# Performance work log

Hardware: AMD Instinct MI355X
Metric: run time of the kernel (lower is better)

## Reference

```python
import jax, jax.numpy as jnp
import numpy as np

EPS = 1e-5
SCALE = 30.0

def _ln(x, g, b):
    m = jnp.mean(x, axis=-1, keepdims=True)
    v = jnp.mean((x - m) ** 2, axis=-1, keepdims=True)
    return (x - m) * jax.lax.rsqrt(v + EPS) * g + b

def setup_inputs() -> dict:
    key = jax.random.key(0)
    ks = jax.random.split(key, 12)
    B, L, K, H, NIN = 4, 2048, 48, 128, 512
    s = 0.02
    return {
        "h_V": jax.random.normal(ks[0], (B, L, H), jnp.float32),
        "h_E": jax.random.normal(ks[1], (B, L, K, NIN - H), jnp.float32),
        "mask_V": jnp.ones((B, L), jnp.float32),
        "mask_E": jnp.ones((B, L, K), jnp.float32),
        "w1": jax.random.normal(ks[2], (NIN, H), jnp.float32) * s,
        "b1": jnp.zeros((H,), jnp.float32),
        "w2": jax.random.normal(ks[3], (H, H), jnp.float32) * s,
        "b2": jnp.zeros((H,), jnp.float32),
        "w3": jax.random.normal(ks[4], (H, H), jnp.float32) * s,
        "b3": jnp.zeros((H,), jnp.float32),
        "g1": jnp.ones((H,), jnp.float32),
        "bn1": jnp.zeros((H,), jnp.float32),
        "g2": jnp.ones((H,), jnp.float32),
        "bn2": jnp.zeros((H,), jnp.float32),
        "wf1": jax.random.normal(ks[5], (H, 4 * H), jnp.float32) * s,
        "bf1": jnp.zeros((4 * H,), jnp.float32),
        "wf2": jax.random.normal(ks[6], (4 * H, H), jnp.float32) * s,
        "bf2": jnp.zeros((H,), jnp.float32),
    }

def reference(h_V, h_E, mask_V, mask_E, w1, b1, w2, b2, w3, b3, g1, bn1, g2, bn2, wf1, bf1, wf2, bf2):
    B, L, H = h_V.shape
    K = h_E.shape[-2]
    gelu = lambda x: jax.nn.gelu(x, approximate=False)  # torch nn.GELU default (erf)
    # expand source node over K neighbors and concat: (B,L,K,num_in)
    h_V_exp = jnp.broadcast_to(h_V[:, :, None, :], (B, L, K, H))
    h_EV = jnp.concatenate([h_V_exp, h_E], axis=-1)
    h_msg = gelu(jnp.einsum('blki,ih->blkh', h_EV, w1) + b1)
    h_msg = gelu(jnp.einsum('blkh,hj->blkj', h_msg, w2) + b2)
    h_msg = jnp.einsum('blkh,hj->blkj', h_msg, w3) + b3
    h_msg = mask_E[..., None] * h_msg
    dh = jnp.sum(h_msg, axis=-2) / SCALE  # masked sum-aggregate over K
    h = _ln(h_V + dh, g1, bn1)
    dff = jnp.einsum('blh,hf->blf', h, wf1) + bf1
    dff = jnp.einsum('blf,fh->blh', gelu(dff), wf2) + bf2
    h = _ln(h + dff, g2, bn2)
    return mask_V[..., None] * h
```

## Files before the change

kernel.cpp:

```cpp
#include <hip/hip_runtime.h>
#include <hip/hip_bf16.h>


typedef __bf16 bf16x8 __attribute__((ext_vector_type(8)));
typedef __bf16 bf16x4 __attribute__((ext_vector_type(4)));
typedef float f32x4 __attribute__((ext_vector_type(4)));

#define HH 128
#define EE 384
#define KK 48

__device__ __forceinline__ float gelu_f(float x) {
  float x2 = x * x;
  float u = x * (-1.5957691216f - 0.0713548163f * x2);
  float e = __expf(u);
  return __fdividef(x, 1.0f + e);
}

__device__ __forceinline__ bf16x8 cvt8v(f32x4 a, f32x4 b) {
  bf16x8 r;
  #pragma unroll
  for (int i = 0; i < 4; ++i) { r[i] = (__bf16)a[i]; r[i + 4] = (__bf16)b[i]; }
  return r;
}

__device__ __forceinline__ f32x4 mfma16(bf16x8 a, bf16x8 b, f32x4 c) {
  return __builtin_amdgcn_mfma_f32_16x16x32_bf16(a, b, c, 0, 0, 0);
}

__device__ __forceinline__ void gload16(const void* g, void* l) {
  __builtin_amdgcn_global_load_lds(
      (const __attribute__((address_space(1))) void*)g,
      (__attribute__((address_space(3))) void*)l, 16, 0, 0);
}

__global__ void prep_kernel(const float* __restrict__ w1, const float* __restrict__ w2,
                            const float* __restrict__ w3, const float* __restrict__ wf1,
                            const float* __restrict__ wf2, __bf16* __restrict__ out) {
  int idx = blockIdx.x * 256 + threadIdx.x;
  if (idx < 49152) {
    int t = idx & 7, lane = (idx >> 3) & 63, n = (idx >> 9) & 7, kc = idx >> 12;
    int e = kc * 32 + (lane >> 4) * 8 + t, h = n * 16 + (lane & 15);
    out[idx] = (__bf16)w1[(128 + e) * 128 + h];
  } else if (idx < 65536) {
    int u = idx - 49152;
    int t = u & 7, lane = (u >> 3) & 63, n = (u >> 9) & 7, kc = u >> 12;
    int e = kc * 32 + (lane >> 4) * 8 + t, h = n * 16 + (lane & 15);
    out[idx] = (__bf16)w2[e * 128 + h];
  } else if (idx < 81920) {
    int u = idx - 65536;
    int t = u & 7, lane = (u >> 3) & 63, n = (u >> 9) & 7, kc = u >> 12;
    int e = kc * 32 + (lane >> 4) * 8 + t, h = n * 16 + (lane & 15);
    out[idx] = (__bf16)w3[e * 128 + h];
  } else if (idx < 147456) {
    int u = idx - 81920;
    int t = u & 7, lane = (u >> 3) & 63, n = (u >> 9) & 7, kc = (u >> 12) & 3, w = u >> 14;
    int f = w * 128 + n * 16 + (lane & 15), h = kc * 32 + (lane >> 4) * 8 + t;
    out[idx] = (__bf16)wf1[h * 512 + f];
  } else if (idx < 212992) {
    int u = idx - 147456;
    int t = u & 7, lane = (u >> 3) & 63, n = (u >> 9) & 1, kc = (u >> 10) & 15, w = u >> 14;
    int j = w * 32 + n * 16 + (lane & 15), f = kc * 32 + (lane >> 4) * 8 + t;
    out[idx] = (__bf16)wf2[f * 128 + j];
  }
}

__global__ __launch_bounds__(128) void v1_kernel(const float* __restrict__ hV,
                                                 const float* __restrict__ w1,
                                                 const float* __restrict__ b1,
                                                 float* __restrict__ V1) {
  __shared__ __align__(16) float sV[16][128];
  const int tid = threadIdx.x;
  const long p0 = (long)blockIdx.x * 16;
  for (int i = 0; i < 16; ++i) sV[i][tid] = hV[(p0 + i) * HH + tid];
  __syncthreads();
  float acc[16];
  float bb = b1[tid];
  #pragma unroll
  for (int p = 0; p < 16; ++p) acc[p] = bb;
  for (int k = 0; k < 128; k += 4) {
    float wa = w1[(k + 0) * HH + tid];
    float wb = w1[(k + 1) * HH + tid];
    float wc = w1[(k + 2) * HH + tid];
    float wd = w1[(k + 3) * HH + tid];
    #pragma unroll
    for (int p = 0; p < 16; ++p) {
      float4 h4 = *(const float4*)&sV[p][k];
      acc[p] = fmaf(h4.x, wa, fmaf(h4.y, wb, fmaf(h4.z, wc, fmaf(h4.w, wd, acc[p]))));
    }
  }
  #pragma unroll
  for (int p = 0; p < 16; ++p) V1[(p0 + p) * HH + tid] = acc[p];
}

__global__ __launch_bounds__(256, 2) void msg_kernel(
    const float* __restrict__ hE, const float* __restrict__ hV,
    const float* __restrict__ maskE,
    const __bf16* __restrict__ w1f, const __bf16* __restrict__ w2f,
    const __bf16* __restrict__ w3f, const float* __restrict__ V1,
    const float* __restrict__ b2, const float* __restrict__ b3,
    const float* __restrict__ g1, const float* __restrict__ bn1,
    float* __restrict__ outH) {
  __shared__ __align__(16) float sStage[4][4608];

  const int tid = threadIdx.x;
  const int lane = tid & 63;
  const int w = tid >> 6;
  const long p = (long)blockIdx.x * 4 + w;
  const int fr = lane & 15;
  const int fg = lane >> 4;
  char* stDst = (char*)&sStage[w][0];
  const int swz = (fr & 7) << 4;

  const int r_l = lane >> 3;
  const int cswz = ((lane & 7) ^ r_l) * 16;
  const char* gA = (const char*)(hE + p * KK * (long)EE) + r_l * (EE * 4) + cswz;

  const __bf16* b1p = w1f + lane * 8;
  const __bf16* b2p = w2f + lane * 8;
  const __bf16* b3p = w3f + lane * 8;

  f32x4 acc[3][8];
  #pragma unroll
  for (int m = 0; m < 3; ++m)
    #pragma unroll
    for (int n = 0; n < 8; ++n) acc[m][n] = (f32x4){0.f, 0.f, 0.f, 0.f};

  bf16x8 BsA[8], BsB[8];

#define STAGEA(KC, BUFI) { \
    _Pragma("unroll") for (int q_ = 0; q_ < 6; ++q_) \
      gload16(gA + (KC) * 128 + q_ * (8 * EE * 4), stDst + (BUFI) * 6144 + q_ * 1024); }
#define LOADB(BUF, BP, KC) { \
    _Pragma("unroll") for (int n_ = 0; n_ < 8; ++n_) \
      BUF[n_] = *(const bf16x8*)((BP) + ((KC) * 8 + n_) * 512); }
#define WAITV(N) asm volatile("s_waitcnt vmcnt(" #N ")" ::: "memory")

#define GITER(WAITN, BUFI, BUSE, DOSTAGE, STKC, STBUF, DOB, BLP, BLKC) { \
    WAITV(WAITN); \
    const char* rb_ = stDst + (BUFI) * 6144; \
    f32x4 x0_ = *(const f32x4*)(rb_ + fr * 128 + ((fg * 32) ^ swz)); \
    f32x4 x1_ = *(const f32x4*)(rb_ + fr * 128 + ((fg * 32 + 16) ^ swz)); \
    f32x4 x2_ = *(const f32x4*)(rb_ + (16 + fr) * 128 + ((fg * 32) ^ swz)); \
    f32x4 x3_ = *(const f32x4*)(rb_ + (16 + fr) * 128 + ((fg * 32 + 16) ^ swz)); \
    f32x4 x4_ = *(const f32x4*)(rb_ + (32 + fr) * 128 + ((fg * 32) ^ swz)); \
    f32x4 x5_ = *(const f32x4*)(rb_ + (32 + fr) * 128 + ((fg * 32 + 16) ^ swz)); \
    if (DOSTAGE) STAGEA(STKC, STBUF); \
    bf16x8 af0 = cvt8v(x0_, x1_); \
    bf16x8 af1 = cvt8v(x2_, x3_); \
    bf16x8 af2 = cvt8v(x4_, x5_); \
    _Pragma("unroll") for (int n_ = 0; n_ < 8; ++n_) { \
      acc[0][n_] = mfma16(BUSE[n_], af0, acc[0][n_]); \
      acc[1][n_] = mfma16(BUSE[n_], af1, acc[1][n_]); \
      acc[2][n_] = mfma16(BUSE[n_], af2, acc[2][n_]); } \
    if (DOB) LOADB(BUSE, BLP, BLKC); }

#define STEPL(BUSE, KC, DOB, BLP, BLKC) { \
    const int cb_ = (((KC) * 64 + fg * 16) ^ swz); \
    bf16x8 af0 = *(const bf16x8*)(stDst + fr * 256 + cb_); \
    bf16x8 af1 = *(const bf16x8*)(stDst + (16 + fr) * 256 + cb_); \
    bf16x8 af2 = *(const bf16x8*)(stDst + (32 + fr) * 256 + cb_); \
    _Pragma("unroll") for (int n_ = 0; n_ < 8; ++n_) { \
      acc[0][n_] = mfma16(BUSE[n_], af0, acc[0][n_]); \
      acc[1][n_] = mfma16(BUSE[n_], af1, acc[1][n_]); \
      acc[2][n_] = mfma16(BUSE[n_], af2, acc[2][n_]); } \
    if (DOB) LOADB(BUSE, BLP, BLKC); }

#define EPI(BIASQ) { \
    _Pragma("unroll") for (int m_ = 0; m_ < 3; ++m_) { \
      const int rb_ = (m_ * 16 + fr) * 256; \
      _Pragma("unroll") for (int n_ = 0; n_ < 8; ++n_) { \
        bf16x4 t_; \
        _Pragma("unroll") for (int j_ = 0; j_ < 4; ++j_) \
          t_[j_] = (__bf16)gelu_f(acc[m_][n_][j_] + BIASQ[n_][j_]); \
        *(bf16x4*)(stDst + rb_ + ((n_ * 32 + fg * 8) ^ swz)) = t_; \
        acc[m_][n_] = (f32x4){0.f, 0.f, 0.f, 0.f}; } } }

  STAGEA(0, 0);
  LOADB(BsA, b1p, 0);
  STAGEA(1, 1);
  LOADB(BsB, b1p, 1);

  GITER(14, 0, BsA, 1, 2, 2, 1, b1p, 2);
  GITER(14, 1, BsB, 1, 3, 0, 1, b1p, 3);
  GITER(14, 2, BsA, 1, 4, 1, 1, b1p, 4);
  GITER(14, 0, BsB, 1, 5, 2, 1, b1p, 5);
  GITER(14, 1, BsA, 1, 6, 0, 1, b1p, 6);
  GITER(14, 2, BsB, 1, 7, 1, 1, b1p, 7);
  GITER(14, 0, BsA, 1, 8, 2, 1, b1p, 8);
  GITER(14, 1, BsB, 1, 9, 0, 1, b1p, 9);
  GITER(14, 2, BsA, 1, 10, 1, 1, b1p, 10);
  GITER(14, 0, BsB, 1, 11, 2, 1, b1p, 11);

  f32x4 vq[8];
  #pragma unroll
  for (int n = 0; n < 8; ++n) vq[n] = *(const f32x4*)(V1 + p * HH + n * 16 + fg * 4);

  GITER(22, 1, BsA, 0, 0, 0, 1, b2p, 0);
  GITER(16, 2, BsB, 0, 0, 0, 1, b2p, 1);

  EPI(vq);

  { WAITV(8);  STEPL(BsA, 0, 1, b2p, 2); }
  { WAITV(8);  STEPL(BsB, 1, 1, b2p, 3); }
  { WAITV(8);  STEPL(BsA, 2, 1, b3p, 0); }
  { WAITV(8);  STEPL(BsB, 3, 1, b3p, 1); }
  {
    f32x4 bq[8];
    #pragma unroll
    for (int n = 0; n < 8; ++n) bq[n] = *(const f32x4*)(b2 + n * 16 + fg * 4);
    EPI(bq);
  }

  { STEPL(BsA, 0, 1, b3p, 2); }
  { STEPL(BsB, 1, 1, b3p, 3); }
  { WAITV(8);  STEPL(BsA, 2, 0, b3p, 0); }
  { WAITV(0);  STEPL(BsB, 3, 0, b3p, 0); }

  const float mk0 = maskE[p * KK + fr];
  const float mk1 = maskE[p * KK + 16 + fr];
  const float mk2 = maskE[p * KK + 32 + fr];
  f32x4 red[8];
  {
    #pragma unroll
    for (int n = 0; n < 8; ++n) {
      f32x4 bq = *(const f32x4*)(b3 + n * 16 + fg * 4);
      red[n] = mk0 * (acc[0][n] + bq) + mk1 * (acc[1][n] + bq) + mk2 * (acc[2][n] + bq);
    }
    #pragma unroll
    for (int off = 1; off <= 8; off <<= 1)
      #pragma unroll
      for (int n = 0; n < 8; ++n)
        #pragma unroll
        for (int j = 0; j < 4; ++j)
          red[n][j] += __shfl_xor(red[n][j], off);
  }

  {
    f32x4 xq[8];
    #pragma unroll
    for (int n = 0; n < 8; ++n)
      xq[n] = *(const f32x4*)(hV + p * HH + n * 16 + fg * 4) + red[n] * (1.f / 30.f);
    float s = 0.f;
    #pragma unroll
    for (int n = 0; n < 8; ++n)
      #pragma unroll
      for (int j = 0; j < 4; ++j) s += xq[n][j];
    s += __shfl_xor(s, 16); s += __shfl_xor(s, 32);
    float mean = s * (1.f / 128.f);
    float qv = 0.f;
    #pragma unroll
    for (int n = 0; n < 8; ++n)
      #pragma unroll
      for (int j = 0; j < 4; ++j) { float e = xq[n][j] - mean; qv += e * e; }
    qv += __shfl_xor(qv, 16); qv += __shfl_xor(qv, 32);
    float rs = rsqrtf(qv * (1.f / 128.f) + 1e-5f);
    if (fr == 0) {
      #pragma unroll
      for (int n = 0; n < 8; ++n) {
        f32x4 gq = *(const f32x4*)(g1 + n * 16 + fg * 4);
        f32x4 bq = *(const f32x4*)(bn1 + n * 16 + fg * 4);
        f32x4 o;
        #pragma unroll
        for (int j = 0; j < 4; ++j) o[j] = (xq[n][j] - mean) * rs * gq[j] + bq[j];
        *(f32x4*)(outH + p * HH + n * 16 + fg * 4) = o;
      }
    }
  }
#undef STAGEA
#undef LOADB
#undef WAITV
#undef GITER
#undef STEPL
#undef EPI
}

__global__ __launch_bounds__(256, 2) void ffn_kernel(
    const float* __restrict__ xin, const __bf16* __restrict__ wf1g,
    const float* __restrict__ bf1, const __bf16* __restrict__ wf2g,
    const float* __restrict__ bf2, const float* __restrict__ g2,
    const float* __restrict__ bn2, const float* __restrict__ maskV,
    float* __restrict__ out) {
  __shared__ __align__(16) __bf16 sX[16][136];
  __shared__ __align__(16) __bf16 sH1[16][520];
  __shared__ __align__(16) float sOut[16][132];
  const int tid = threadIdx.x, lane = tid & 63, w = tid >> 6;
  const long row0 = (long)blockIdx.x * 16;
  const int fr = lane & 15, fg = lane >> 4;
  const __bf16* bw1 = wf1g + w * 16384 + lane * 8;
  const __bf16* bw2 = wf2g + w * 16384 + lane * 8;

  {
    int r = tid >> 4, c = (tid & 15) * 8;
    const float* src = xin + (row0 + r) * HH + c;
    f32x4 v0 = *(const f32x4*)src, v1 = *(const f32x4*)(src + 4);
    *(bf16x8*)&sX[r][c] = cvt8v(v0, v1);
  }
  __syncthreads();

  f32x4 a1[8];
  #pragma unroll
  for (int n = 0; n < 8; ++n) a1[n] = (f32x4){0.f, 0.f, 0.f, 0.f};
  #pragma unroll
  for (int kc = 0; kc < 4; ++kc) {
    int k0 = kc * 32;
    bf16x8 af0 = *(const bf16x8*)&sX[fr][k0 + fg * 8];
    #pragma unroll
    for (int n = 0; n < 8; ++n) {
      bf16x8 bfr = *(const bf16x8*)(bw1 + (kc * 8 + n) * 512);
      a1[n] = mfma16(af0, bfr, a1[n]);
    }
  }
  #pragma unroll
  for (int n = 0; n < 8; ++n) {
    float bv = bf1[w * 128 + n * 16 + fr];
    #pragma unroll
    for (int j = 0; j < 4; ++j)
      sH1[fg * 4 + j][w * 128 + n * 16 + fr] = (__bf16)gelu_f(a1[n][j] + bv);
  }
  __syncthreads();

  f32x4 a2[2];
  #pragma unroll
  for (int n = 0; n < 2; ++n) a2[n] = (f32x4){0.f, 0.f, 0.f, 0.f};
  #pragma unroll
  for (int kc = 0; kc < 16; ++kc) {
    int k0 = kc * 32;
    bf16x8 af0 = *(const bf16x8*)&sH1[fr][k0 + fg * 8];
    #pragma unroll
    for (int n = 0; n < 2; ++n) {
      bf16x8 bfr = *(const bf16x8*)(bw2 + (kc * 2 + n) * 512);
      a2[n] = mfma16(af0, bfr, a2[n]);
    }
  }
  #pragma unroll
  for (int n = 0; n < 2; ++n) {
    float bv = bf2[w * 32 + n * 16 + fr];
    #pragma unroll
    for (int j = 0; j < 4; ++j)
      sOut[fg * 4 + j][w * 32 + n * 16 + fr] = a2[n][j] + bv;
  }
  __syncthreads();

  {
    int r = tid >> 4, c0 = (tid & 15) * 8;
    long p = row0 + r;
    const float* xp = xin + p * HH + c0;
    float x[8];
    #pragma unroll
    for (int i = 0; i < 8; ++i) x[i] = xp[i] + sOut[r][c0 + i];
    float s = 0.f;
    #pragma unroll
    for (int i = 0; i < 8; ++i) s += x[i];
    s += __shfl_xor(s, 1); s += __shfl_xor(s, 2); s += __shfl_xor(s, 4); s += __shfl_xor(s, 8);
    float mean = s * (1.f / 128.f);
    float q = 0.f;
    #pragma unroll
    for (int i = 0; i < 8; ++i) { float e = x[i] - mean; q += e * e; }
    q += __shfl_xor(q, 1); q += __shfl_xor(q, 2); q += __shfl_xor(q, 4); q += __shfl_xor(q, 8);
    float rs = rsqrtf(q * (1.f / 128.f) + 1e-5f);
    float mv = maskV[p];
    float* op = out + p * HH + c0;
    #pragma unroll
    for (int i = 0; i < 8; ++i)
      op[i] = ((x[i] - mean) * rs * g2[c0 + i] + bn2[c0 + i]) * mv;
  }
}

extern "C" void kernel_launch(void* const* d_in, const int* in_sizes, int n_in,
                              void* d_out, int out_size, void* d_ws, size_t ws_size,
                              hipStream_t stream) {
  const float* hV    = (const float*)d_in[0];
  const float* hE    = (const float*)d_in[1];
  const float* maskV = (const float*)d_in[2];
  const float* maskE = (const float*)d_in[3];
  const float* w1    = (const float*)d_in[4];
  const float* b1    = (const float*)d_in[5];
  const float* w2    = (const float*)d_in[6];
  const float* b2    = (const float*)d_in[7];
  const float* w3    = (const float*)d_in[8];
  const float* b3    = (const float*)d_in[9];
  const float* g1    = (const float*)d_in[10];
  const float* bn1   = (const float*)d_in[11];
  const float* g2    = (const float*)d_in[12];
  const float* bn2   = (const float*)d_in[13];
  const float* wf1   = (const float*)d_in[14];
  const float* bf1   = (const float*)d_in[15];
  const float* wf2   = (const float*)d_in[16];
  const float* bf2   = (const float*)d_in[17];
  float* out = (float*)d_out;

  __bf16* wsb = (__bf16*)d_ws;
  float* V1   = (float*)((char*)d_ws + 425984);
  float* hbuf = (float*)((char*)d_ws + 4620288);

  prep_kernel<<<832, 256, 0, stream>>>(w1, w2, w3, wf1, wf2, wsb);
  v1_kernel<<<512, 128, 0, stream>>>(hV, w1, b1, V1);
  msg_kernel<<<2048, 256, 0, stream>>>(hE, hV, maskE,
                                       wsb, wsb + 49152, wsb + 65536, V1,
                                       b2, b3, g1, bn1, hbuf);
  ffn_kernel<<<512, 256, 0, stream>>>(hbuf, wsb + 81920, bf1, wsb + 147456, bf2,
                                      g2, bn2, maskV, out);
}
```

Measured before the change: 206.2 us.

## Split each node's message MLP across four waves by output columns

The message kernel now assigns one node per block instead of one node per wave. The four waves cooperatively stage the shared hE tile and each computes a 32-column slice of the hidden outputs, with LDS barriers between layers and a cross-wave LayerNorm reduction. Biases are cached in shared memory, per-thread register pressure drops, and launch bounds rise to three blocks per CU with four times as many blocks. The cost is extra barriers per layer, shared-memory round trips of intermediate activations across waves, and a single-pass variance that is less numerically robust.

```diff
diff --git a/kernel.cpp b/kernel.cpp
--- a/kernel.cpp
+++ b/kernel.cpp
@@ -93,7 +93,7 @@
   for (int p = 0; p < 16; ++p) V1[(p0 + p) * HH + tid] = acc[p];
 }
 
-__global__ __launch_bounds__(256, 2) void msg_kernel(
+__global__ __launch_bounds__(256, 3) void msg_kernel(
     const float* __restrict__ hE, const float* __restrict__ hV,
     const float* __restrict__ maskE,
     const __bf16* __restrict__ w1f, const __bf16* __restrict__ w2f,
@@ -101,177 +101,227 @@
     const float* __restrict__ b2, const float* __restrict__ b3,
     const float* __restrict__ g1, const float* __restrict__ bn1,
     float* __restrict__ outH) {
-  __shared__ __align__(16) float sStage[4][4608];
+  __shared__ __align__(16) char sBuf[3][12288];
+  __shared__ __align__(16) float sBias[512];
+  __shared__ __align__(16) float sPart[4][2];
 
   const int tid = threadIdx.x;
   const int lane = tid & 63;
   const int w = tid >> 6;
-  const long p = (long)blockIdx.x * 4 + w;
   const int fr = lane & 15;
   const int fg = lane >> 4;
-  char* stDst = (char*)&sStage[w][0];
-  const int swz = (fr & 7) << 4;
-
-  const int r_l = lane >> 3;
-  const int cswz = ((lane & 7) ^ r_l) * 16;
-  const char* gA = (const char*)(hE + p * KK * (long)EE) + r_l * (EE * 4) + cswz;
-
-  const __bf16* b1p = w1f + lane * 8;
-  const __bf16* b2p = w2f + lane * 8;
-  const __bf16* b3p = w3f + lane * 8;
-
-  f32x4 acc[3][8];
+  const long p = blockIdx.x;
+
+  for (int j = tid; j < 512; j += 256) {
+    float v;
+    if (j < 128) v = b2[j];
+    else if (j < 256) v = b3[j - 128];
+    else if (j < 384) v = g1[j - 256];
+    else v = bn1[j - 384];
+    sBias[j] = v;
+  }
+  __syncthreads();
+
+  const float mk0 = maskE[p * KK + fr];
+  const float mk1 = maskE[p * KK + 16 + fr];
+  const float mk2 = maskE[p * KK + 32 + fr];
+
+  const char* hEp = (const char*)(hE + p * (long)(KK * EE));
+  const int lrow = lane >> 4;
+  const int lcb = (lane & 15) * 16;
+  const int r0 = (w * 3 + 0) * 4 + lrow;
+  const int r1 = (w * 3 + 1) * 4 + lrow;
+  const int r2 = (w * 3 + 2) * 4 + lrow;
+  const char* srcA0 = hEp + r0 * 1536 + (lcb ^ ((r0 & 7) << 5));
+  const char* srcA1 = hEp + r1 * 1536 + (lcb ^ ((r1 & 7) << 5));
+  const char* srcA2 = hEp + r2 * 1536 + (lcb ^ ((r2 & 7) << 5));
+  const int dst0 = (w * 3 + 0) * 1024;
+  const int dst1 = (w * 3 + 1) * 1024;
+  const int dst2 = (w * 3 + 2) * 1024;
+
+  const __bf16* b1base = w1f + (2 * w) * 512 + lane * 8;
+  const __bf16* b2base = w2f + (2 * w) * 512 + lane * 8;
+  const __bf16* b3base = w3f + (2 * w) * 512 + lane * 8;
+
+  const int aswz = (fr & 7) << 5;
+  const int hswz = (fr & 7) << 4;
+  char* hB = &sBuf[0][0];
+
+  f32x4 acc[3][2];
   #pragma unroll
   for (int m = 0; m < 3; ++m)
     #pragma unroll
-    for (int n = 0; n < 8; ++n) acc[m][n] = (f32x4){0.f, 0.f, 0.f, 0.f};
-
-  bf16x8 BsA[8], BsB[8];
-
-#define STAGEA(KC, BUFI) { \
-    _Pragma("unroll") for (int q_ = 0; q_ < 6; ++q_) \
-      gload16(gA + (KC) * 128 + q_ * (8 * EE * 4), stDst + (BUFI) * 6144 + q_ * 1024); }
-#define LOADB(BUF, BP, KC) { \
-    _Pragma("unroll") for (int n_ = 0; n_ < 8; ++n_) \
-      BUF[n_] = *(const bf16x8*)((BP) + ((KC) * 8 + n_) * 512); }
+    for (int n = 0; n < 2; ++n) acc[m][n] = (f32x4){0.f, 0.f, 0.f, 0.f};
+
+  bf16x8 Bs0[2], Bs1[2], Bs2[2], Bs3[2];
+
+#define STAGE(C, BUF) { \
+    gload16(srcA0 + (C) * 256, &sBuf[BUF][0] + dst0); \
+    gload16(srcA1 + (C) * 256, &sBuf[BUF][0] + dst1); \
+    gload16(srcA2 + (C) * 256, &sBuf[BUF][0] + dst2); }
+#define LOADB(SET, BASE, KC) { \
+    SET[0] = *(const bf16x8*)((BASE) + (KC) * 4096); \
+    SET[1] = *(const bf16x8*)((BASE) + (KC) * 4096 + 256); }
 #define WAITV(N) asm volatile("s_waitcnt vmcnt(" #N ")" ::: "memory")
-
-#define GITER(WAITN, BUFI, BUSE, DOSTAGE, STKC, STBUF, DOB, BLP, BLKC) { \
-    WAITV(WAITN); \
-    const char* rb_ = stDst + (BUFI) * 6144; \
-    f32x4 x0_ = *(const f32x4*)(rb_ + fr * 128 + ((fg * 32) ^ swz)); \
-    f32x4 x1_ = *(const f32x4*)(rb_ + fr * 128 + ((fg * 32 + 16) ^ swz)); \
-    f32x4 x2_ = *(const f32x4*)(rb_ + (16 + fr) * 128 + ((fg * 32) ^ swz)); \
-    f32x4 x3_ = *(const f32x4*)(rb_ + (16 + fr) * 128 + ((fg * 32 + 16) ^ swz)); \
-    f32x4 x4_ = *(const f32x4*)(rb_ + (32 + fr) * 128 + ((fg * 32) ^ swz)); \
-    f32x4 x5_ = *(const f32x4*)(rb_ + (32 + fr) * 128 + ((fg * 32 + 16) ^ swz)); \
-    if (DOSTAGE) STAGEA(STKC, STBUF); \
+#define BAR      asm volatile("s_barrier" ::: "memory")
+#define BARL     asm volatile("s_waitcnt lgkmcnt(0)\ns_barrier" ::: "memory")
+
+#define KSTEP(BUF, KS, SET) { \
+    const char* rb_ = &sBuf[BUF][0]; \
+    const int cb_ = ((KS) * 128 + fg * 32) ^ aswz; \
+    f32x4 x0_ = *(const f32x4*)(rb_ + fr * 256 + cb_); \
+    f32x4 x1_ = *(const f32x4*)(rb_ + fr * 256 + cb_ + 16); \
+    f32x4 x2_ = *(const f32x4*)(rb_ + (16 + fr) * 256 + cb_); \
+    f32x4 x3_ = *(const f32x4*)(rb_ + (16 + fr) * 256 + cb_ + 16); \
+    f32x4 x4_ = *(const f32x4*)(rb_ + (32 + fr) * 256 + cb_); \
+    f32x4 x5_ = *(const f32x4*)(rb_ + (32 + fr) * 256 + cb_ + 16); \
     bf16x8 af0 = cvt8v(x0_, x1_); \
     bf16x8 af1 = cvt8v(x2_, x3_); \
     bf16x8 af2 = cvt8v(x4_, x5_); \
-    _Pragma("unroll") for (int n_ = 0; n_ < 8; ++n_) { \
-      acc[0][n_] = mfma16(BUSE[n_], af0, acc[0][n_]); \
-      acc[1][n_] = mfma16(BUSE[n_], af1, acc[1][n_]); \
-      acc[2][n_] = mfma16(BUSE[n_], af2, acc[2][n_]); } \
-    if (DOB) LOADB(BUSE, BLP, BLKC); }
-
-#define STEPL(BUSE, KC, DOB, BLP, BLKC) { \
-    const int cb_ = (((KC) * 64 + fg * 16) ^ swz); \
-    bf16x8 af0 = *(const bf16x8*)(stDst + fr * 256 + cb_); \
-    bf16x8 af1 = *(const bf16x8*)(stDst + (16 + fr) * 256 + cb_); \
-    bf16x8 af2 = *(const bf16x8*)(stDst + (32 + fr) * 256 + cb_); \
-    _Pragma("unroll") for (int n_ = 0; n_ < 8; ++n_) { \
-      acc[0][n_] = mfma16(BUSE[n_], af0, acc[0][n_]); \
-      acc[1][n_] = mfma16(BUSE[n_], af1, acc[1][n_]); \
-      acc[2][n_] = mfma16(BUSE[n_], af2, acc[2][n_]); } \
-    if (DOB) LOADB(BUSE, BLP, BLKC); }
-
-#define EPI(BIASQ) { \
+    acc[0][0] = mfma16(SET[0], af0, acc[0][0]); acc[0][1] = mfma16(SET[1], af0, acc[0][1]); \
+    acc[1][0] = mfma16(SET[0], af1, acc[1][0]); acc[1][1] = mfma16(SET[1], af1, acc[1][1]); \
+    acc[2][0] = mfma16(SET[0], af2, acc[2][0]); acc[2][1] = mfma16(SET[1], af2, acc[2][1]); }
+
+#define KSTEPH(KS, SET) { \
+    const int cb_ = ((KS) * 64 + fg * 16) ^ hswz; \
+    bf16x8 af0 = *(const bf16x8*)(hB + fr * 256 + cb_); \
+    bf16x8 af1 = *(const bf16x8*)(hB + (16 + fr) * 256 + cb_); \
+    bf16x8 af2 = *(const bf16x8*)(hB + (32 + fr) * 256 + cb_); \
+    acc[0][0] = mfma16(SET[0], af0, acc[0][0]); acc[0][1] = mfma16(SET[1], af0, acc[0][1]); \
+    acc[1][0] = mfma16(SET[0], af1, acc[1][0]); acc[1][1] = mfma16(SET[1], af1, acc[1][1]); \
+    acc[2][0] = mfma16(SET[0], af2, acc[2][0]); acc[2][1] = mfma16(SET[1], af2, acc[2][1]); }
+
+#define EPI(BQ0, BQ1) { \
     _Pragma("unroll") for (int m_ = 0; m_ < 3; ++m_) { \
       const int rb_ = (m_ * 16 + fr) * 256; \
-      _Pragma("unroll") for (int n_ = 0; n_ < 8; ++n_) { \
-        bf16x4 t_; \
-        _Pragma("unroll") for (int j_ = 0; j_ < 4; ++j_) \
-          t_[j_] = (__bf16)gelu_f(acc[m_][n_][j_] + BIASQ[n_][j_]); \
-        *(bf16x4*)(stDst + rb_ + ((n_ * 32 + fg * 8) ^ swz)) = t_; \
-        acc[m_][n_] = (f32x4){0.f, 0.f, 0.f, 0.f}; } } }
-
-  STAGEA(0, 0);
-  LOADB(BsA, b1p, 0);
-  STAGEA(1, 1);
-  LOADB(BsB, b1p, 1);
-
-  GITER(14, 0, BsA, 1, 2, 2, 1, b1p, 2);
-  GITER(14, 1, BsB, 1, 3, 0, 1, b1p, 3);
-  GITER(14, 2, BsA, 1, 4, 1, 1, b1p, 4);
-  GITER(14, 0, BsB, 1, 5, 2, 1, b1p, 5);
-  GITER(14, 1, BsA, 1, 6, 0, 1, b1p, 6);
-  GITER(14, 2, BsB, 1, 7, 1, 1, b1p, 7);
-  GITER(14, 0, BsA, 1, 8, 2, 1, b1p, 8);
-  GITER(14, 1, BsB, 1, 9, 0, 1, b1p, 9);
-  GITER(14, 2, BsA, 1, 10, 1, 1, b1p, 10);
-  GITER(14, 0, BsB, 1, 11, 2, 1, b1p, 11);
-
-  f32x4 vq[8];
-  #pragma unroll
-  for (int n = 0; n < 8; ++n) vq[n] = *(const f32x4*)(V1 + p * HH + n * 16 + fg * 4);
-
-  GITER(22, 1, BsA, 0, 0, 0, 1, b2p, 0);
-  GITER(16, 2, BsB, 0, 0, 0, 1, b2p, 1);
-
-  EPI(vq);
-
-  { WAITV(8);  STEPL(BsA, 0, 1, b2p, 2); }
-  { WAITV(8);  STEPL(BsB, 1, 1, b2p, 3); }
-  { WAITV(8);  STEPL(BsA, 2, 1, b3p, 0); }
-  { WAITV(8);  STEPL(BsB, 3, 1, b3p, 1); }
+      { bf16x4 t_; \
+        _Pragma("unroll") for (int j_ = 0; j_ < 4; ++j_) t_[j_] = (__bf16)gelu_f(acc[m_][0][j_] + BQ0[j_]); \
+        *(bf16x4*)(hB + rb_ + (((2 * w) * 32 + fg * 8) ^ hswz)) = t_; \
+        acc[m_][0] = (f32x4){0.f, 0.f, 0.f, 0.f}; } \
+      { bf16x4 t_; \
+        _Pragma("unroll") for (int j_ = 0; j_ < 4; ++j_) t_[j_] = (__bf16)gelu_f(acc[m_][1][j_] + BQ1[j_]); \
+        *(bf16x4*)(hB + rb_ + (((2 * w + 1) * 32 + fg * 8) ^ hswz)) = t_; \
+        acc[m_][1] = (f32x4){0.f, 0.f, 0.f, 0.f}; } } }
+
+  STAGE(0, 0);
+  LOADB(Bs0, b1base, 0);
+  LOADB(Bs1, b1base, 1);
+  STAGE(1, 1);
+  LOADB(Bs2, b1base, 2);
+  LOADB(Bs3, b1base, 3);
+
+  f32x4 vq0, vq1, hq0, hq1;
+
+  WAITV(7); BAR;
+  KSTEP(0, 0, Bs0); LOADB(Bs0, b1base, 4);
+  KSTEP(0, 1, Bs1); LOADB(Bs1, b1base, 5);
+  STAGE(2, 2);
+
+  WAITV(7); BAR;
+  KSTEP(1, 0, Bs2); LOADB(Bs2, b1base, 6);
+  KSTEP(1, 1, Bs3); LOADB(Bs3, b1base, 7);
+  STAGE(3, 0);
+
+  WAITV(7); BAR;
+  KSTEP(2, 0, Bs0); LOADB(Bs0, b1base, 8);
+  KSTEP(2, 1, Bs1); LOADB(Bs1, b1base, 9);
+  STAGE(4, 1);
+
+  WAITV(7); BAR;
+  KSTEP(0, 0, Bs2); LOADB(Bs2, b1base, 10);
+  KSTEP(0, 1, Bs3); LOADB(Bs3, b1base, 11);
+  STAGE(5, 2);
+
+  WAITV(7); BAR;
+  KSTEP(1, 0, Bs0); LOADB(Bs0, b2base, 0);
+  vq0 = *(const f32x4*)(V1 + p * HH + (2 * w) * 16 + fg * 4);
+  vq1 = *(const f32x4*)(V1 + p * HH + (2 * w + 1) * 16 + fg * 4);
+  KSTEP(1, 1, Bs1); LOADB(Bs1, b2base, 1);
+
+  WAITV(6); BAR;
+  KSTEP(2, 0, Bs2); LOADB(Bs2, b2base, 2);
+  KSTEP(2, 1, Bs3); LOADB(Bs3, b2base, 3);
+
+  WAITV(4);
+  EPI(vq0, vq1);
+  BARL;
+
+  KSTEPH(0, Bs0); LOADB(Bs0, b3base, 0);
+  KSTEPH(1, Bs1); LOADB(Bs1, b3base, 1);
+  WAITV(4);
+  KSTEPH(2, Bs2); LOADB(Bs2, b3base, 2);
+  KSTEPH(3, Bs3); LOADB(Bs3, b3base, 3);
+  BARL;
   {
-    f32x4 bq[8];
-    #pragma unroll
-    for (int n = 0; n < 8; ++n) bq[n] = *(const f32x4*)(b2 + n * 16 + fg * 4);
-    EPI(bq);
-  }
-
-  { STEPL(BsA, 0, 1, b3p, 2); }
-  { STEPL(BsB, 1, 1, b3p, 3); }
-  { WAITV(8);  STEPL(BsA, 2, 0, b3p, 0); }
-  { WAITV(0);  STEPL(BsB, 3, 0, b3p, 0); }
-
-  const float mk0 = maskE[p * KK + fr];
-  const float mk1 = maskE[p * KK + 16 + fr];
-  const float mk2 = maskE[p * KK + 32 + fr];
-  f32x4 red[8];
+    f32x4 bq0 = *(const f32x4*)(&sBias[(2 * w) * 16 + fg * 4]);
+    f32x4 bq1 = *(const f32x4*)(&sBias[(2 * w + 1) * 16 + fg * 4]);
+    EPI(bq0, bq1);
+  }
+  BARL;
+
+  WAITV(6);
+  KSTEPH(0, Bs0);
+  hq0 = *(const f32x4*)(hV + p * HH + (2 * w) * 16 + fg * 4);
+  hq1 = *(const f32x4*)(hV + p * HH + (2 * w + 1) * 16 + fg * 4);
+  KSTEPH(1, Bs1);
+  WAITV(4);
+  KSTEPH(2, Bs2);
+  KSTEPH(3, Bs3);
+
+  f32x4 red[2];
   {
     #pragma unroll
-    for (int n = 0; n < 8; ++n) {
-      f32x4 bq = *(const f32x4*)(b3 + n * 16 + fg * 4);
+    for (int n = 0; n < 2; ++n) {
+      f32x4 bq = *(const f32x4*)(&sBias[128 + (2 * w + n) * 16 + fg * 4]);
       red[n] = mk0 * (acc[0][n] + bq) + mk1 * (acc[1][n] + bq) + mk2 * (acc[2][n] + bq);
     }
     #pragma unroll
     for (int off = 1; off <= 8; off <<= 1)
       #pragma unroll
-      for (int n = 0; n < 8; ++n)
+      for (int n = 0; n < 2; ++n)
         #pragma unroll
         for (int j = 0; j < 4; ++j)
           red[n][j] += __shfl_xor(red[n][j], off);
   }
 
+  WAITV(0);
   {
-    f32x4 xq[8];
-    #pragma unroll
-    for (int n = 0; n < 8; ++n)
-      xq[n] = *(const f32x4*)(hV + p * HH + n * 16 + fg * 4) + red[n] * (1.f / 30.f);
-    float s = 0.f;
-    #pragma unroll
-    for (int n = 0; n < 8; ++n)
+    f32x4 xq[2];
+    xq[0] = hq0 + red[0] * (1.f / 30.f);
+    xq[1] = hq1 + red[1] * (1.f / 30.f);
+    float s = 0.f, t = 0.f;
+    #pragma unroll
+    for (int n = 0; n < 2; ++n)
       #pragma unroll
-      for (int j = 0; j < 4; ++j) s += xq[n][j];
+      for (int j = 0; j < 4; ++j) { float x = xq[n][j]; s += x; t += x * x; }
     s += __shfl_xor(s, 16); s += __shfl_xor(s, 32);
-    float mean = s * (1.f / 128.f);
-    float qv = 0.f;
-    #pragma unroll
-    for (int n = 0; n < 8; ++n)
-      #pragma unroll
-      for (int j = 0; j < 4; ++j) { float e = xq[n][j] - mean; qv += e * e; }
-    qv += __shfl_xor(qv, 16); qv += __shfl_xor(qv, 32);
-    float rs = rsqrtf(qv * (1.f / 128.f) + 1e-5f);
+    t += __shfl_xor(t, 16); t += __shfl_xor(t, 32);
+    if (lane == 0) { sPart[w][0] = s; sPart[w][1] = t; }
+    BARL;
+    float S = sPart[0][0] + sPart[1][0] + sPart[2][0] + sPart[3][0];
+    float T = sPart[0][1] + sPart[1][1] + sPart[2][1] + sPart[3][1];
+    float mean = S * (1.f / 128.f);
+    float var = T * (1.f / 128.f) - mean * mean;
+    float rs = rsqrtf(var + 1e-5f);
     if (fr == 0) {
       #pragma unroll
-      for (int n = 0; n < 8; ++n) {
-        f32x4 gq = *(const f32x4*)(g1 + n * 16 + fg * 4);
-        f32x4 bq = *(const f32x4*)(bn1 + n * 16 + fg * 4);
+      for (int n = 0; n < 2; ++n) {
+        f32x4 gq = *(const f32x4*)(&sBias[256 + (2 * w + n) * 16 + fg * 4]);
+        f32x4 bq = *(const f32x4*)(&sBias[384 + (2 * w + n) * 16 + fg * 4]);
         f32x4 o;
         #pragma unroll
         for (int j = 0; j < 4; ++j) o[j] = (xq[n][j] - mean) * rs * gq[j] + bq[j];
-        *(f32x4*)(outH + p * HH + n * 16 + fg * 4) = o;
+        *(f32x4*)(outH + p * HH + (2 * w + n) * 16 + fg * 4) = o;
       }
     }
   }
-#undef STAGEA
+#undef STAGE
 #undef LOADB
 #undef WAITV
-#undef GITER
-#undef STEPL
+#undef BAR
+#undef BARL
+#undef KSTEP
+#undef KSTEPH
 #undef EPI
 }
 
@@ -396,7 +446,7 @@
 
   prep_kernel<<<832, 256, 0, stream>>>(w1, w2, w3, wf1, wf2, wsb);
   v1_kernel<<<512, 128, 0, stream>>>(hV, w1, b1, V1);
-  msg_kernel<<<2048, 256, 0, stream>>>(hE, hV, maskE,
+  msg_kernel<<<8192, 256, 0, stream>>>(hE, hV, maskE,
                                        wsb, wsb + 49152, wsb + 65536, V1,
                                        b2, b3, g1, bn1, hbuf);
   ffn_kernel<<<512, 256, 0, stream>>>(hbuf, wsb + 81920, bf1, wsb + 147456, bf2,
```

Result: faster. 201.5 us (-2.2%).

## Split each node's 48 neighbors across three waves with LDS cross-wave reduction

Applied to the files above, without the earlier changes.

The message kernel now assigns one node per 192-thread block, with each wave handling 16 of the 48 neighbor rows instead of one wave processing all 48. The cross-wave sum goes through shared memory with a barrier, and one wave does the layer norm. Biases are staged in LDS, and V1/hV are fetched asynchronously into LDS with 4-byte global_load_lds. The staging ring is deepened to six slots. This cuts per-wave accumulator registers from 3x8 to 8 tiles to raise occupancy and latency hiding. In exchange, each block reloads the weight fragments, adds a barrier, and leaves two waves idle during the final normalization.

```diff
diff --git a/kernel.cpp b/kernel.cpp
--- a/kernel.cpp
+++ b/kernel.cpp
@@ -32,6 +32,11 @@
   __builtin_amdgcn_global_load_lds(
       (const __attribute__((address_space(1))) void*)g,
       (__attribute__((address_space(3))) void*)l, 16, 0, 0);
+}
+__device__ __forceinline__ void gload4(const void* g, void* l) {
+  __builtin_amdgcn_global_load_lds(
+      (const __attribute__((address_space(1))) void*)g,
+      (__attribute__((address_space(3))) void*)l, 4, 0, 0);
 }
 
 __global__ void prep_kernel(const float* __restrict__ w1, const float* __restrict__ w2,
@@ -93,7 +98,7 @@
   for (int p = 0; p < 16; ++p) V1[(p0 + p) * HH + tid] = acc[p];
 }
 
-__global__ __launch_bounds__(256, 2) void msg_kernel(
+__global__ __launch_bounds__(192, 3) void msg_kernel(
     const float* __restrict__ hE, const float* __restrict__ hV,
     const float* __restrict__ maskE,
     const __bf16* __restrict__ w1f, const __bf16* __restrict__ w2f,
@@ -101,131 +106,147 @@
     const float* __restrict__ b2, const float* __restrict__ b3,
     const float* __restrict__ g1, const float* __restrict__ bn1,
     float* __restrict__ outH) {
-  __shared__ __align__(16) float sStage[4][4608];
+  __shared__ __align__(16) char sA[3][12288];
+  __shared__ __align__(16) float sAux[3][256];
+  __shared__ __align__(16) float sBias[512];
+  __shared__ __align__(16) float sDH[3][128];
 
   const int tid = threadIdx.x;
   const int lane = tid & 63;
   const int w = tid >> 6;
-  const long p = (long)blockIdx.x * 4 + w;
   const int fr = lane & 15;
   const int fg = lane >> 4;
-  char* stDst = (char*)&sStage[w][0];
+  const long p = blockIdx.x;
+
+  for (int j = tid; j < 512; j += 192) {
+    float v;
+    if (j < 128) v = b2[j];
+    else if (j < 256) v = b3[j - 128];
+    else if (j < 384) v = g1[j - 256];
+    else v = bn1[j - 384];
+    sBias[j] = v;
+  }
+  __syncthreads();
+
+  const float mk = maskE[p * KK + 16 * w + fr];
+
+  const char* baseA = (const char*)(hE + p * (long)(KK * EE)) + (16 * w) * 1536;
+  const int lperm = ((lane & 7) ^ (lane >> 3)) << 4;
+  const char* src0 = baseA + (lane >> 3) * 1536 + lperm;
+  const char* src1 = baseA + 8 * 1536 + (lane >> 3) * 1536 + lperm;
+  char* sAw = &sA[w][0];
+  char* auxw = (char*)&sAux[w][0];
   const int swz = (fr & 7) << 4;
-
-  const int r_l = lane >> 3;
-  const int cswz = ((lane & 7) ^ r_l) * 16;
-  const char* gA = (const char*)(hE + p * KK * (long)EE) + r_l * (EE * 4) + cswz;
 
   const __bf16* b1p = w1f + lane * 8;
   const __bf16* b2p = w2f + lane * 8;
   const __bf16* b3p = w3f + lane * 8;
 
-  f32x4 acc[3][8];
-  #pragma unroll
-  for (int m = 0; m < 3; ++m)
-    #pragma unroll
-    for (int n = 0; n < 8; ++n) acc[m][n] = (f32x4){0.f, 0.f, 0.f, 0.f};
-
-  bf16x8 BsA[8], BsB[8];
-
-#define STAGEA(KC, BUFI) { \
-    _Pragma("unroll") for (int q_ = 0; q_ < 6; ++q_) \
-      gload16(gA + (KC) * 128 + q_ * (8 * EE * 4), stDst + (BUFI) * 6144 + q_ * 1024); }
-#define LOADB(BUF, BP, KC) { \
+  f32x4 acc[8];
+  #pragma unroll
+  for (int n = 0; n < 8; ++n) acc[n] = (f32x4){0.f, 0.f, 0.f, 0.f};
+
+  bf16x8 BA[8], BB[8];
+
+#define STAGE(C) { \
+    gload16(src0 + (C) * 128, sAw + ((C) % 6) * 2048); \
+    gload16(src1 + (C) * 128, sAw + ((C) % 6) * 2048 + 1024); }
+#define LOADB8(SET, BP, KC) { \
     _Pragma("unroll") for (int n_ = 0; n_ < 8; ++n_) \
-      BUF[n_] = *(const bf16x8*)((BP) + ((KC) * 8 + n_) * 512); }
+      SET[n_] = *(const bf16x8*)((BP) + ((KC) * 8 + n_) * 512); }
 #define WAITV(N) asm volatile("s_waitcnt vmcnt(" #N ")" ::: "memory")
 
-#define GITER(WAITN, BUFI, BUSE, DOSTAGE, STKC, STBUF, DOB, BLP, BLKC) { \
-    WAITV(WAITN); \
-    const char* rb_ = stDst + (BUFI) * 6144; \
-    f32x4 x0_ = *(const f32x4*)(rb_ + fr * 128 + ((fg * 32) ^ swz)); \
-    f32x4 x1_ = *(const f32x4*)(rb_ + fr * 128 + ((fg * 32 + 16) ^ swz)); \
-    f32x4 x2_ = *(const f32x4*)(rb_ + (16 + fr) * 128 + ((fg * 32) ^ swz)); \
-    f32x4 x3_ = *(const f32x4*)(rb_ + (16 + fr) * 128 + ((fg * 32 + 16) ^ swz)); \
-    f32x4 x4_ = *(const f32x4*)(rb_ + (32 + fr) * 128 + ((fg * 32) ^ swz)); \
-    f32x4 x5_ = *(const f32x4*)(rb_ + (32 + fr) * 128 + ((fg * 32 + 16) ^ swz)); \
-    if (DOSTAGE) STAGEA(STKC, STBUF); \
-    bf16x8 af0 = cvt8v(x0_, x1_); \
-    bf16x8 af1 = cvt8v(x2_, x3_); \
-    bf16x8 af2 = cvt8v(x4_, x5_); \
+#define G1STEP(WN, SLOT, BUSE, DOST, STC, BLP, BLKC) { \
+    WAITV(WN); \
+    const char* rb_ = sAw + (SLOT) * 2048 + fr * 128; \
+    f32x4 x0_ = *(const f32x4*)(rb_ + ((fg * 32) ^ swz)); \
+    f32x4 x1_ = *(const f32x4*)(rb_ + ((fg * 32 + 16) ^ swz)); \
+    if (DOST) STAGE(STC); \
+    bf16x8 af_ = cvt8v(x0_, x1_); \
+    _Pragma("unroll") for (int n_ = 0; n_ < 8; ++n_) \
+      acc[n_] = mfma16(BUSE[n_], af_, acc[n_]); \
+    LOADB8(BUSE, BLP, BLKC); }
+
+#define GHSTEP(WN, HOFF, KS, BUSE, DOB, BLP, BLKC) { \
+    WAITV(WN); \
+    bf16x8 af_ = *(const bf16x8*)(sAw + (HOFF) + fr * 256 + (((KS) * 64 + fg * 16) ^ swz)); \
+    _Pragma("unroll") for (int n_ = 0; n_ < 8; ++n_) \
+      acc[n_] = mfma16(BUSE[n_], af_, acc[n_]); \
+    if (DOB) LOADB8(BUSE, BLP, BLKC); }
+
+#define EPIH(HOFF, BQ) { \
     _Pragma("unroll") for (int n_ = 0; n_ < 8; ++n_) { \
-      acc[0][n_] = mfma16(BUSE[n_], af0, acc[0][n_]); \
-      acc[1][n_] = mfma16(BUSE[n_], af1, acc[1][n_]); \
-      acc[2][n_] = mfma16(BUSE[n_], af2, acc[2][n_]); } \
-    if (DOB) LOADB(BUSE, BLP, BLKC); }
-
-#define STEPL(BUSE, KC, DOB, BLP, BLKC) { \
-    const int cb_ = (((KC) * 64 + fg * 16) ^ swz); \
-    bf16x8 af0 = *(const bf16x8*)(stDst + fr * 256 + cb_); \
-    bf16x8 af1 = *(const bf16x8*)(stDst + (16 + fr) * 256 + cb_); \
-    bf16x8 af2 = *(const bf16x8*)(stDst + (32 + fr) * 256 + cb_); \
-    _Pragma("unroll") for (int n_ = 0; n_ < 8; ++n_) { \
-      acc[0][n_] = mfma16(BUSE[n_], af0, acc[0][n_]); \
-      acc[1][n_] = mfma16(BUSE[n_], af1, acc[1][n_]); \
-      acc[2][n_] = mfma16(BUSE[n_], af2, acc[2][n_]); } \
-    if (DOB) LOADB(BUSE, BLP, BLKC); }
-
-#define EPI(BIASQ) { \
-    _Pragma("unroll") for (int m_ = 0; m_ < 3; ++m_) { \
-      const int rb_ = (m_ * 16 + fr) * 256; \
-      _Pragma("unroll") for (int n_ = 0; n_ < 8; ++n_) { \
-        bf16x4 t_; \
-        _Pragma("unroll") for (int j_ = 0; j_ < 4; ++j_) \
-          t_[j_] = (__bf16)gelu_f(acc[m_][n_][j_] + BIASQ[n_][j_]); \
-        *(bf16x4*)(stDst + rb_ + ((n_ * 32 + fg * 8) ^ swz)) = t_; \
-        acc[m_][n_] = (f32x4){0.f, 0.f, 0.f, 0.f}; } } }
-
-  STAGEA(0, 0);
-  LOADB(BsA, b1p, 0);
-  STAGEA(1, 1);
-  LOADB(BsB, b1p, 1);
-
-  GITER(14, 0, BsA, 1, 2, 2, 1, b1p, 2);
-  GITER(14, 1, BsB, 1, 3, 0, 1, b1p, 3);
-  GITER(14, 2, BsA, 1, 4, 1, 1, b1p, 4);
-  GITER(14, 0, BsB, 1, 5, 2, 1, b1p, 5);
-  GITER(14, 1, BsA, 1, 6, 0, 1, b1p, 6);
-  GITER(14, 2, BsB, 1, 7, 1, 1, b1p, 7);
-  GITER(14, 0, BsA, 1, 8, 2, 1, b1p, 8);
-  GITER(14, 1, BsB, 1, 9, 0, 1, b1p, 9);
-  GITER(14, 2, BsA, 1, 10, 1, 1, b1p, 10);
-  GITER(14, 0, BsB, 1, 11, 2, 1, b1p, 11);
-
-  f32x4 vq[8];
-  #pragma unroll
-  for (int n = 0; n < 8; ++n) vq[n] = *(const f32x4*)(V1 + p * HH + n * 16 + fg * 4);
-
-  GITER(22, 1, BsA, 0, 0, 0, 1, b2p, 0);
-  GITER(16, 2, BsB, 0, 0, 0, 1, b2p, 1);
-
-  EPI(vq);
-
-  { WAITV(8);  STEPL(BsA, 0, 1, b2p, 2); }
-  { WAITV(8);  STEPL(BsB, 1, 1, b2p, 3); }
-  { WAITV(8);  STEPL(BsA, 2, 1, b3p, 0); }
-  { WAITV(8);  STEPL(BsB, 3, 1, b3p, 1); }
+      bf16x4 t_; \
+      _Pragma("unroll") for (int j_ = 0; j_ < 4; ++j_) \
+        t_[j_] = (__bf16)gelu_f(acc[n_][j_] + BQ[n_][j_]); \
+      *(bf16x4*)(sAw + (HOFF) + fr * 256 + ((n_ * 32 + fg * 8) ^ swz)) = t_; \
+      acc[n_] = (f32x4){0.f, 0.f, 0.f, 0.f}; } }
+
+  STAGE(0); STAGE(1); STAGE(2); STAGE(3); STAGE(4);
+  LOADB8(BA, b1p, 0);
+  LOADB8(BB, b1p, 1);
+
+  G1STEP(8,  0, BA, 1, 5,  b1p, 2);
+  G1STEP(10, 1, BB, 1, 6,  b1p, 3);
+  G1STEP(10, 2, BA, 1, 7,  b1p, 4);
+  G1STEP(10, 3, BB, 1, 8,  b1p, 5);
+  G1STEP(10, 4, BA, 1, 9,  b1p, 6);
+  G1STEP(10, 5, BB, 1, 10, b1p, 7);
+  G1STEP(10, 0, BA, 1, 11, b1p, 8);
+  G1STEP(10, 1, BB, 0, 0,  b1p, 9);
+  G1STEP(8,  2, BA, 0, 0,  b1p, 10);
+  G1STEP(8,  3, BB, 0, 0,  b1p, 11);
+  {
+    WAITV(8);
+    const char* rb_ = sAw + 4 * 2048 + fr * 128;
+    f32x4 x0_ = *(const f32x4*)(rb_ + ((fg * 32) ^ swz));
+    f32x4 x1_ = *(const f32x4*)(rb_ + ((fg * 32 + 16) ^ swz));
+    bf16x8 af_ = cvt8v(x0_, x1_);
+    #pragma unroll
+    for (int n_ = 0; n_ < 8; ++n_) acc[n_] = mfma16(BA[n_], af_, acc[n_]);
+    LOADB8(BA, b2p, 0);
+    gload4(V1 + p * HH + lane, auxw);
+    gload4(V1 + p * HH + 64 + lane, auxw + 256);
+  }
+  G1STEP(10, 5, BB, 0, 0, b2p, 1);
+
+  WAITV(8);
+  {
+    f32x4 vq[8];
+    #pragma unroll
+    for (int n = 0; n < 8; ++n) vq[n] = *(const f32x4*)(auxw + (n * 16 + fg * 4) * 4);
+    EPIH(0, vq);
+  }
+
+  GHSTEP(8, 0, 0, BA, 1, b2p, 2);
+  GHSTEP(8, 0, 1, BB, 1, b2p, 3);
+  GHSTEP(8, 0, 2, BA, 1, b3p, 0);
+  GHSTEP(8, 0, 3, BB, 1, b3p, 1);
   {
     f32x4 bq[8];
     #pragma unroll
-    for (int n = 0; n < 8; ++n) bq[n] = *(const f32x4*)(b2 + n * 16 + fg * 4);
-    EPI(bq);
-  }
-
-  { STEPL(BsA, 0, 1, b3p, 2); }
-  { STEPL(BsB, 1, 1, b3p, 3); }
-  { WAITV(8);  STEPL(BsA, 2, 0, b3p, 0); }
-  { WAITV(0);  STEPL(BsB, 3, 0, b3p, 0); }
-
-  const float mk0 = maskE[p * KK + fr];
-  const float mk1 = maskE[p * KK + 16 + fr];
-  const float mk2 = maskE[p * KK + 32 + fr];
-  f32x4 red[8];
-  {
+    for (int n = 0; n < 8; ++n) bq[n] = *(const f32x4*)(&sBias[n * 16 + fg * 4]);
+    EPIH(4096, bq);
+  }
+
+  GHSTEP(8, 4096, 0, BA, 1, b3p, 2);
+  GHSTEP(8, 4096, 1, BB, 1, b3p, 3);
+  {
+    WAITV(8);
+    bf16x8 af_ = *(const bf16x8*)(sAw + 4096 + fr * 256 + ((2 * 64 + fg * 16) ^ swz));
+    #pragma unroll
+    for (int n_ = 0; n_ < 8; ++n_) acc[n_] = mfma16(BA[n_], af_, acc[n_]);
+    gload4(hV + p * HH + lane, auxw + 512);
+    gload4(hV + p * HH + 64 + lane, auxw + 768);
+  }
+  GHSTEP(2, 4096, 3, BB, 0, b3p, 0);
+
+  {
+    f32x4 red[8];
     #pragma unroll
     for (int n = 0; n < 8; ++n) {
-      f32x4 bq = *(const f32x4*)(b3 + n * 16 + fg * 4);
-      red[n] = mk0 * (acc[0][n] + bq) + mk1 * (acc[1][n] + bq) + mk2 * (acc[2][n] + bq);
+      f32x4 bq = *(const f32x4*)(&sBias[128 + n * 16 + fg * 4]);
+      red[n] = mk * (acc[n] + bq);
     }
     #pragma unroll
     for (int off = 1; off <= 8; off <<= 1)
@@ -234,13 +255,25 @@
         #pragma unroll
         for (int j = 0; j < 4; ++j)
           red[n][j] += __shfl_xor(red[n][j], off);
-  }
-
-  {
+    if (fr == 0) {
+      #pragma unroll
+      for (int n = 0; n < 8; ++n)
+        *(f32x4*)(&sDH[w][n * 16 + fg * 4]) = red[n];
+    }
+  }
+  asm volatile("s_waitcnt lgkmcnt(0)\ns_barrier" ::: "memory");
+
+  if (w == 0) {
+    WAITV(0);
     f32x4 xq[8];
     #pragma unroll
-    for (int n = 0; n < 8; ++n)
-      xq[n] = *(const f32x4*)(hV + p * HH + n * 16 + fg * 4) + red[n] * (1.f / 30.f);
+    for (int n = 0; n < 8; ++n) {
+      f32x4 d0 = *(const f32x4*)(&sDH[0][n * 16 + fg * 4]);
+      f32x4 d1 = *(const f32x4*)(&sDH[1][n * 16 + fg * 4]);
+      f32x4 d2 = *(const f32x4*)(&sDH[2][n * 16 + fg * 4]);
+      f32x4 hq = *(const f32x4*)(auxw + (128 + n * 16 + fg * 4) * 4);
+      xq[n] = hq + (d0 + d1 + d2) * (1.f / 30.f);
+    }
     float s = 0.f;
     #pragma unroll
     for (int n = 0; n < 8; ++n)
@@ -258,8 +291,8 @@
     if (fr == 0) {
       #pragma unroll
       for (int n = 0; n < 8; ++n) {
-        f32x4 gq = *(const f32x4*)(g1 + n * 16 + fg * 4);
-        f32x4 bq = *(const f32x4*)(bn1 + n * 16 + fg * 4);
+        f32x4 gq = *(const f32x4*)(&sBias[256 + n * 16 + fg * 4]);
+        f32x4 bq = *(const f32x4*)(&sBias[384 + n * 16 + fg * 4]);
         f32x4 o;
         #pragma unroll
         for (int j = 0; j < 4; ++j) o[j] = (xq[n][j] - mean) * rs * gq[j] + bq[j];
@@ -267,12 +300,12 @@
       }
     }
   }
-#undef STAGEA
-#undef LOADB
+#undef STAGE
+#undef LOADB8
 #undef WAITV
-#undef GITER
-#undef STEPL
-#undef EPI
+#undef G1STEP
+#undef GHSTEP
+#undef EPIH
 }
 
 __global__ __launch_bounds__(256, 2) void ffn_kernel(
@@ -396,7 +429,7 @@
 
   prep_kernel<<<832, 256, 0, stream>>>(w1, w2, w3, wf1, wf2, wsb);
   v1_kernel<<<512, 128, 0, stream>>>(hV, w1, b1, V1);
-  msg_kernel<<<2048, 256, 0, stream>>>(hE, hV, maskE,
+  msg_kernel<<<8192, 192, 0, stream>>>(hE, hV, maskE,
                                        wsb, wsb + 49152, wsb + 65536, V1,
                                        b2, b3, g1, bn1, hbuf);
   ffn_kernel<<<512, 256, 0, stream>>>(hbuf, wsb + 81920, bf1, wsb + 147456, bf2,
```

After: 301.6 us. 46.3% more time.
